# Performance work log

Measured on AMD Instinct MI355X. Metric: run time of the kernel, lower is better.

## Reference

```python
import jax, jax.numpy as jnp
import numpy as np

T, N, G, H, E = 20, 256, 8, 128, 64
G2 = G * G


def setup_inputs() -> dict:
    key = jax.random.key(0)
    ks = jax.random.split(key, 16)
    scene = jax.random.normal(ks[0], (T, N, 3), dtype=jnp.float32)
    grids = (jax.random.uniform(ks[1], (T, N, N, G2)) < 0.05).astype(jnp.float32)
    hidden_states = jax.random.normal(ks[2], (N, H), dtype=jnp.float32) * 0.1
    cell_states = jax.random.normal(ks[3], (N, H), dtype=jnp.float32) * 0.1
    dimensions = jnp.array([640, 480], dtype=jnp.int64)
    s = lambda fan: 1.0 / np.sqrt(fan)
    W_in = jax.random.normal(ks[4], (E, 2), dtype=jnp.float32) * s(2)
    b_in = jnp.zeros((E,), dtype=jnp.float32)
    W_t = jax.random.normal(ks[5], (E, G2 * H), dtype=jnp.float32) * s(G2 * H)
    b_t = jnp.zeros((E,), dtype=jnp.float32)
    W_ih = jax.random.normal(ks[6], (4 * H, 2 * E), dtype=jnp.float32) * s(2 * E)
    b_ih = jnp.zeros((4 * H,), dtype=jnp.float32)
    W_hh = jax.random.normal(ks[7], (4 * H, H), dtype=jnp.float32) * s(H)
    b_hh = jnp.zeros((4 * H,), dtype=jnp.float32)
    W_out = jax.random.normal(ks[8], (5, H), dtype=jnp.float32) * s(H)
    b_out = jnp.zeros((5,), dtype=jnp.float32)
    return {"scene": scene, "grids": grids, "hidden_states": hidden_states,
            "cell_states": cell_states, "dimensions": dimensions,
            "W_in": W_in, "b_in": b_in, "W_t": W_t, "b_t": b_t,
            "W_ih": W_ih, "b_ih": b_ih, "W_hh": W_hh, "b_hh": b_hh,
            "W_out": W_out, "b_out": b_out}


def reference(scene, grids, hidden_states, cell_states, dimensions,
              W_in, b_in, W_t, b_t, W_ih, b_ih, W_hh, b_hh, W_out, b_out):
    # dimensions is unused by forward() (only by infer()), kept for signature fidelity.
    xy_seq = scene[:, :, 1:3]  # [T, N, 2]

    def step(carry, xs):
        h, c = carry                      # [N, H] each
        xy, grid = xs                     # [N, 2], [N, N, G2]
        # social pooling: for each ped p, grid[p]^T @ h  -> [G2, H]
        social = jnp.einsum('pog,oh->pgh', grid, h).reshape(grid.shape[0], G2 * H)
        inp_emb = jax.nn.relu(xy @ W_in.T + b_in)         # [N, E] (dropout in eval mode)
        ten_emb = jax.nn.relu(social @ W_t.T + b_t)       # [N, E]
        x = jnp.concatenate([inp_emb, ten_emb], axis=1)   # [N, 2E]
        gates = x @ W_ih.T + b_ih + h @ W_hh.T + b_hh     # [N, 4H]
        i, f, g, o = jnp.split(gates, 4, axis=1)          # PyTorch LSTMCell gate order
        c2 = jax.nn.sigmoid(f) * c + jax.nn.sigmoid(i) * jnp.tanh(g)
        h2 = jax.nn.sigmoid(o) * jnp.tanh(c2)
        out = h2 @ W_out.T + b_out                        # [N, 5]
        return (h2, c2), out

    (h_fin, c_fin), outputs = jax.lax.scan(step, (hidden_states, cell_states), (xy_seq, grids))
    return outputs, h_fin, c_fin
```

## Files before the change

### kernel.cpp

```cpp
#include <hip/hip_runtime.h>
#include <cstdint>
#include <cstddef>

#define T_STEPS 20
#define N_PED   256
#define G2C     64
#define HDIM    128
#define EDIM    64
#define NG      16384

__device__ __forceinline__ int swz(int row, int hd) {
    return row * 128 + ((((hd >> 2) ^ (row & 31)) << 2) | (hd & 3));
}

__global__ __launch_bounds__(256) void kP(
    const float* __restrict__ scene, const float* __restrict__ hidden,
    const float* __restrict__ cell,  const float* __restrict__ W_in,
    const float* __restrict__ b_in,  const float* __restrict__ W_ih,
    const float* __restrict__ b_ih,  const float* __restrict__ b_hh,
    float* __restrict__ pg, float* __restrict__ h0, float* __restrict__ c0,
    float* __restrict__ W_ihT)
{
    int bid = blockIdx.x, tid = threadIdx.x;
    if (bid >= 1280) {
        int gid = (bid - 1280) * 256 + tid;
        for (int u = gid; u < 32768; u += 4096) {
            h0[u] = hidden[u];
            c0[u] = cell[u];
            int e = u >> 9, j = u & 511;
            W_ihT[u] = W_ih[j * 128 + 64 + e];
        }
        return;
    }
    __shared__ float ie[16 * 64];
    __shared__ float wih[128 * 65];
    int tb = bid >> 6;
    int p0 = ((bid >> 2) & 15) * 16;
    int j0 = (bid & 3) * 128;

    for (int k = 0; k < 8; ++k) {
        int f4 = tid + k * 256;
        int fl = f4 * 4;
        int j_loc = fl >> 6, e0 = fl & 63;
        float4 v = *(const float4*)(W_ih + (size_t)(j0 + j_loc) * 128 + e0);
        wih[j_loc * 65 + e0 + 0] = v.x;
        wih[j_loc * 65 + e0 + 1] = v.y;
        wih[j_loc * 65 + e0 + 2] = v.z;
        wih[j_loc * 65 + e0 + 3] = v.w;
    }
    {
        int pp = tid >> 4, e0 = (tid & 15) * 4;
        size_t sbase = ((size_t)tb * N_PED + (p0 + pp)) * 3;
        float x = scene[sbase + 1];
        float y = scene[sbase + 2];
        #pragma unroll
        for (int i = 0; i < 4; ++i) {
            int e = e0 + i;
            float v = b_in[e] + x * W_in[e * 2 + 0] + y * W_in[e * 2 + 1];
            ie[pp * 64 + e] = v > 0.f ? v : 0.f;
        }
    }
    __syncthreads();
    for (int k = 0; k < 8; ++k) {
        int u = k * 256 + tid;
        int pp = u >> 7, j_loc = u & 127;
        int j = j0 + j_loc;
        float s = b_ih[j] + b_hh[j];
        #pragma unroll 8
        for (int e = 0; e < 64; ++e)
            s = fmaf(ie[pp * 64 + e], wih[j_loc * 65 + e], s);
        pg[((size_t)tb * N_PED + (p0 + pp)) * 512 + j] = s;
    }
}

__global__ __launch_bounds__(256) void kC(
    const float* __restrict__ grids, int* __restrict__ counts,
    unsigned short* __restrict__ gidx)
{
    int r = blockIdx.x;
    int tid = threadIdx.x, lane = tid & 63, w = tid >> 6;
    __shared__ unsigned short st[4][1024];
    __shared__ int wcnts[4];
    const float* row = grids + (size_t)r * NG;
    int wcnt = 0;
    for (int rd = 0; rd < 16; ++rd) {
        int fb = w * 4096 + rd * 256 + lane * 4;
        float4 v = *(const float4*)(row + fb);
        #pragma unroll
        for (int c = 0; c < 4; ++c) {
            float val = (c == 0) ? v.x : (c == 1) ? v.y : (c == 2) ? v.z : v.w;
            unsigned long long m = __ballot(val != 0.0f);
            if (val != 0.0f) {
                int pos = wcnt + (int)__popcll(m & ((1ull << lane) - 1ull));
                st[w][pos] = (unsigned short)(fb + c);
            }
            wcnt += (int)__popcll(m);
        }
    }
    if (lane == 0) wcnts[w] = wcnt;
    __syncthreads();
    int base = 0;
    #pragma unroll
    for (int i = 0; i < 4; ++i) if (i < w) base += wcnts[i];
    for (int k = lane; k < wcnt; k += 64)
        gidx[(size_t)r * 1024 + base + k] = st[w][k];
    if (tid == 0) counts[r] = wcnts[0] + wcnts[1] + wcnts[2] + wcnts[3];
}

__global__ __launch_bounds__(256) void k1(
    const float* __restrict__ h, const float* __restrict__ W_t,
    const float* __restrict__ W_hh, float* __restrict__ A,
    float* __restrict__ hhg)
{
    __shared__ float smem[16384];
    float* hs = smem;
    float* wt = smem + 8192;
    int bid = blockIdx.x, tid = threadIdx.x;

    if (bid < 256) {
        int g = bid & 63, o0 = (bid >> 6) * 64;
        for (int k = 0; k < 8; ++k) {
            int fl = (tid + k * 256) * 4;
            int r = fl >> 7, hd = fl & 127;
            float4 v = *(const float4*)(h + (size_t)(o0 + r) * 128 + hd);
            *(float4*)&hs[swz(r, hd)] = v;
            float4 wv = *(const float4*)(W_t + (size_t)r * 8192 + g * 128 + hd);
            *(float4*)&wt[swz(r, hd)] = wv;
        }
        __syncthreads();
        int o_l = (tid >> 4) * 4, e_l = (tid & 15) * 4;
        float acc[4][4] = {};
        for (int hb = 0; hb < 32; ++hb) {
            int hd = hb << 2;
            float4 a[4], b[4];
            #pragma unroll
            for (int i = 0; i < 4; ++i) a[i] = *(float4*)&hs[swz(o_l + i, hd)];
            #pragma unroll
            for (int j = 0; j < 4; ++j) b[j] = *(float4*)&wt[swz(e_l + j, hd)];
            #pragma unroll
            for (int i = 0; i < 4; ++i)
                #pragma unroll
                for (int j = 0; j < 4; ++j) {
                    acc[i][j] = fmaf(a[i].x, b[j].x, acc[i][j]);
                    acc[i][j] = fmaf(a[i].y, b[j].y, acc[i][j]);
                    acc[i][j] = fmaf(a[i].z, b[j].z, acc[i][j]);
                    acc[i][j] = fmaf(a[i].w, b[j].w, acc[i][j]);
                }
        }
        #pragma unroll
        for (int i = 0; i < 4; ++i) {
            float4 r4 = make_float4(acc[i][0], acc[i][1], acc[i][2], acc[i][3]);
            *(float4*)&A[(size_t)(o0 + o_l + i) * 4096 + g * 64 + e_l] = r4;
        }
    } else {
        int hb2 = bid - 256;
        int o0 = (hb2 & 3) * 64, j0 = (hb2 >> 2) * 32;
        for (int k = 0; k < 8; ++k) {
            int fl = (tid + k * 256) * 4;
            int r = fl >> 7, hd = fl & 127;
            float4 v = *(const float4*)(h + (size_t)(o0 + r) * 128 + hd);
            *(float4*)&hs[swz(r, hd)] = v;
        }
        for (int k = 0; k < 4; ++k) {
            int fl = (tid + k * 256) * 4;
            int r = fl >> 7, hd = fl & 127;
            float4 wv = *(const float4*)(W_hh + (size_t)(j0 + r) * 128 + hd);
            *(float4*)&wt[swz(r, hd)] = wv;
        }
        __syncthreads();
        int o_l = (tid >> 4) * 4, j_l = (tid & 15) * 2;
        float acc[4][2] = {};
        for (int hb = 0; hb < 32; ++hb) {
            int hd = hb << 2;
            float4 a[4], b[2];
            #pragma unroll
            for (int i = 0; i < 4; ++i) a[i] = *(float4*)&hs[swz(o_l + i, hd)];
            #pragma unroll
            for (int j = 0; j < 2; ++j) b[j] = *(float4*)&wt[swz(j_l + j, hd)];
            #pragma unroll
            for (int i = 0; i < 4; ++i)
                #pragma unroll
                for (int j = 0; j < 2; ++j) {
                    acc[i][j] = fmaf(a[i].x, b[j].x, acc[i][j]);
                    acc[i][j] = fmaf(a[i].y, b[j].y, acc[i][j]);
                    acc[i][j] = fmaf(a[i].z, b[j].z, acc[i][j]);
                    acc[i][j] = fmaf(a[i].w, b[j].w, acc[i][j]);
                }
        }
        #pragma unroll
        for (int i = 0; i < 4; ++i) {
            float2 r2 = make_float2(acc[i][0], acc[i][1]);
            *(float2*)&hhg[(size_t)(o0 + o_l + i) * 512 + j0 + j_l] = r2;
        }
    }
}

__global__ __launch_bounds__(512) void k2(
    int t, int last, const int* __restrict__ counts,
    const unsigned short* __restrict__ gidx,
    const float* __restrict__ A,     const float* __restrict__ hhg,
    const float* __restrict__ pg,    const float* __restrict__ W_ihT,
    const float* __restrict__ b_t,   const float* __restrict__ W_out,
    const float* __restrict__ b_out, const float* __restrict__ c_cur,
    float* __restrict__ c_next, float* __restrict__ h_next,
    float* __restrict__ out)
{
    int p = blockIdx.x;
    int tid = threadIdx.x, lane = tid & 63, w = tid >> 6;
    __shared__ unsigned short lidx[1024];
    __shared__ float part[8][64];
    __shared__ float ten[64];
    __shared__ float gts[512];
    __shared__ float h2s[128];

    int r = t * N_PED + p;
    int cnt = counts[r];
    ((unsigned int*)lidx)[tid] = ((const unsigned int*)(gidx + (size_t)r * 1024))[tid];
    __syncthreads();

    float acc = 0.f;
    int k = w;
    for (; k + 24 < cnt; k += 32) {
        int i0 = lidx[k], i1 = lidx[k + 8], i2 = lidx[k + 16], i3 = lidx[k + 24];
        float a0 = A[(size_t)i0 * 64 + lane];
        float a1 = A[(size_t)i1 * 64 + lane];
        float a2 = A[(size_t)i2 * 64 + lane];
        float a3 = A[(size_t)i3 * 64 + lane];
        acc += a0; acc += a1; acc += a2; acc += a3;
    }
    for (; k < cnt; k += 8)
        acc += A[(size_t)lidx[k] * 64 + lane];
    part[w][lane] = acc;
    __syncthreads();

    if (tid < 64) {
        float s = b_t[tid];
        #pragma unroll
        for (int ww = 0; ww < 8; ++ww) s += part[ww][tid];
        ten[tid] = s > 0.f ? s : 0.f;
    }
    __syncthreads();

    {
        int j = tid;
        float gj = pg[(size_t)r * 512 + j] + hhg[(size_t)p * 512 + j];
        #pragma unroll 8
        for (int e = 0; e < 64; ++e)
            gj = fmaf(ten[e], W_ihT[e * 512 + j], gj);
        gts[j] = gj;
    }
    __syncthreads();

    if (tid < 128) {
        float ig = gts[tid], fg = gts[128 + tid], gg = gts[256 + tid], og = gts[384 + tid];
        float si = 1.f / (1.f + expf(-ig));
        float sf = 1.f / (1.f + expf(-fg));
        float so = 1.f / (1.f + expf(-og));
        float cold = c_cur[p * 128 + tid];
        float c2 = sf * cold + si * tanhf(gg);
        float h2 = so * tanhf(c2);
        c_next[p * 128 + tid] = c2;
        h_next[p * 128 + tid] = h2;
        h2s[tid] = h2;
        if (last) {
            out[25600 + p * 128 + tid] = h2;
            out[58368 + p * 128 + tid] = c2;
        }
    }
    __syncthreads();

    if (w < 5) {
        float s = h2s[lane] * W_out[w * 128 + lane]
                + h2s[lane + 64] * W_out[w * 128 + 64 + lane];
        #pragma unroll
        for (int off = 32; off > 0; off >>= 1) s += __shfl_xor(s, off);
        if (lane == 0) out[(size_t)r * 5 + w] = s + b_out[w];
    }
}

extern "C" void kernel_launch(void* const* d_in, const int* in_sizes, int n_in,
                              void* d_out, int out_size, void* d_ws, size_t ws_size,
                              hipStream_t stream) {
    (void)in_sizes; (void)n_in; (void)out_size; (void)ws_size;
    const float* scene  = (const float*)d_in[0];
    const float* grids  = (const float*)d_in[1];
    const float* hidden = (const float*)d_in[2];
    const float* cell   = (const float*)d_in[3];
    const float* W_in  = (const float*)d_in[5];
    const float* b_in  = (const float*)d_in[6];
    const float* W_t   = (const float*)d_in[7];
    const float* b_t   = (const float*)d_in[8];
    const float* W_ih  = (const float*)d_in[9];
    const float* b_ih  = (const float*)d_in[10];
    const float* W_hh  = (const float*)d_in[11];
    const float* b_hh  = (const float*)d_in[12];
    const float* W_out = (const float*)d_in[13];
    const float* b_out = (const float*)d_in[14];

    float* ws   = (float*)d_ws;
    float* hbuf = ws;
    float* cbuf = ws + 65536;
    float* A    = ws + 131072;
    float* hhg  = ws + 1179648;
    float* pg   = ws + 1310720;
    float* WT   = ws + 3932160;
    int*   counts = (int*)(ws + 3964928);
    unsigned short* gidx = (unsigned short*)(ws + 3970048);
    float* outf = (float*)d_out;

    hipLaunchKernelGGL(kC, dim3(5120), dim3(256), 0, stream,
                       grids, counts, gidx);
    hipLaunchKernelGGL(kP, dim3(1296), dim3(256), 0, stream,
                       scene, hidden, cell, W_in, b_in, W_ih, b_ih, b_hh,
                       pg, hbuf, cbuf, WT);

    for (int t = 0; t < T_STEPS; ++t) {
        const float* hcur = hbuf + (t & 1) * 32768;
        float*       hnxt = hbuf + ((t + 1) & 1) * 32768;
        const float* ccur = cbuf + (t & 1) * 32768;
        float*       cnxt = cbuf + ((t + 1) & 1) * 32768;
        hipLaunchKernelGGL(k1, dim3(320), dim3(256), 0, stream,
                           hcur, W_t, W_hh, A, hhg);
        hipLaunchKernelGGL(k2, dim3(256), dim3(512), 0, stream,
                           t, (t == T_STEPS - 1) ? 1 : 0,
                           counts, gidx, A, hhg, pg, WT, b_t, W_out, b_out,
                           ccur, cnxt, hnxt, outf);
    }
}
```

Measured before the change: 1.067 ms.

## Fuse per-timestep kernels into one persistent cooperative kernel with grid sync

Replaces the 40 per-step launches (k1 projection GEMM and k2 gather/LSTM) with a single cooperative kernel that loops over all timesteps and separates phases with grid-wide syncs. The h@W_hh term moves from a separate GEMM into the per-pedestrian gate loop, using a W_hhT transposed in the prep kernel. The A GEMM splits the K dimension across warp halves and reduces through shared memory. This is meant to remove launch overhead and inter-kernel gaps, at the cost of grid-sync latency and fewer blocks (256) doing the A GEMM.

New measurement: 2.235 ms. 110% more time.

```diff
diff --git a/kernel.cpp b/kernel.cpp
--- a/kernel.cpp
+++ b/kernel.cpp
@@ -1,16 +1,16 @@
 #include <hip/hip_runtime.h>
+#include <hip/hip_cooperative_groups.h>
 #include <cstdint>
 #include <cstddef>
 
+namespace cg = cooperative_groups;
+
 #define T_STEPS 20
 #define N_PED   256
-#define G2C     64
-#define HDIM    128
-#define EDIM    64
 #define NG      16384
 
-__device__ __forceinline__ int swz(int row, int hd) {
-    return row * 128 + ((((hd >> 2) ^ (row & 31)) << 2) | (hd & 3));
+__device__ __forceinline__ int swz64(int row, int k) {
+    return row * 64 + ((((k >> 2) ^ (row & 15)) << 2) | (k & 3));
 }
 
 __global__ __launch_bounds__(256) void kP(
@@ -18,8 +18,9 @@
     const float* __restrict__ cell,  const float* __restrict__ W_in,
     const float* __restrict__ b_in,  const float* __restrict__ W_ih,
     const float* __restrict__ b_ih,  const float* __restrict__ b_hh,
+    const float* __restrict__ W_hh,
     float* __restrict__ pg, float* __restrict__ h0, float* __restrict__ c0,
-    float* __restrict__ W_ihT)
+    float* __restrict__ W_ihT, float* __restrict__ W_hhT)
 {
     int bid = blockIdx.x, tid = threadIdx.x;
     if (bid >= 1280) {
@@ -30,6 +31,10 @@
             int e = u >> 9, j = u & 511;
             W_ihT[u] = W_ih[j * 128 + 64 + e];
         }
+        for (int u = gid; u < 65536; u += 4096) {
+            int h = u >> 9, j = u & 511;
+            W_hhT[u] = W_hh[j * 128 + h];
+        }
         return;
     }
     __shared__ float ie[16 * 64];
@@ -39,8 +44,7 @@
     int j0 = (bid & 3) * 128;
 
     for (int k = 0; k < 8; ++k) {
-        int f4 = tid + k * 256;
-        int fl = f4 * 4;
+        int fl = (tid + k * 256) * 4;
         int j_loc = fl >> 6, e0 = fl & 63;
         float4 v = *(const float4*)(W_ih + (size_t)(j0 + j_loc) * 128 + e0);
         wih[j_loc * 65 + e0 + 0] = v.x;
@@ -107,174 +111,168 @@
     if (tid == 0) counts[r] = wcnts[0] + wcnts[1] + wcnts[2] + wcnts[3];
 }
 
-__global__ __launch_bounds__(256) void k1(
-    const float* __restrict__ h, const float* __restrict__ W_t,
-    const float* __restrict__ W_hh, float* __restrict__ A,
-    float* __restrict__ hhg)
+__global__ __launch_bounds__(512) void kStep(
+    const int* __restrict__ counts, const unsigned short* __restrict__ gidx,
+    const float* __restrict__ W_t,  const float* __restrict__ pg,
+    const float* __restrict__ W_ihT, const float* __restrict__ W_hhT,
+    const float* __restrict__ b_t,  const float* __restrict__ W_out,
+    const float* __restrict__ b_out,
+    float* __restrict__ hbuf, float* __restrict__ cbuf,
+    float* __restrict__ A, float* __restrict__ out)
 {
+    cg::grid_group gg = cg::this_grid();
     __shared__ float smem[16384];
-    float* hs = smem;
-    float* wt = smem + 8192;
     int bid = blockIdx.x, tid = threadIdx.x;
-
-    if (bid < 256) {
-        int g = bid & 63, o0 = (bid >> 6) * 64;
-        for (int k = 0; k < 8; ++k) {
-            int fl = (tid + k * 256) * 4;
-            int r = fl >> 7, hd = fl & 127;
-            float4 v = *(const float4*)(h + (size_t)(o0 + r) * 128 + hd);
-            *(float4*)&hs[swz(r, hd)] = v;
-            float4 wv = *(const float4*)(W_t + (size_t)r * 8192 + g * 128 + hd);
-            *(float4*)&wt[swz(r, hd)] = wv;
-        }
-        __syncthreads();
-        int o_l = (tid >> 4) * 4, e_l = (tid & 15) * 4;
-        float acc[4][4] = {};
-        for (int hb = 0; hb < 32; ++hb) {
-            int hd = hb << 2;
-            float4 a[4], b[4];
+    int lane = tid & 63, w = tid >> 6;
+
+    for (int t = 0; t < T_STEPS; ++t) {
+        const float* h  = hbuf + (t & 1) * 32768;
+        const float* c  = cbuf + (t & 1) * 32768;
+        float*       hn = hbuf + ((t + 1) & 1) * 32768;
+        float*       cn = cbuf + ((t + 1) & 1) * 32768;
+
+        {
+            int o0 = (bid >> 6) * 64, g = bid & 63;
             #pragma unroll
-            for (int i = 0; i < 4; ++i) a[i] = *(float4*)&hs[swz(o_l + i, hd)];
+            for (int i = 0; i < 8; ++i) {
+                int u = i * 512 + tid;
+                if (u < 2048) {
+                    int kh = u >> 10, rem = u & 1023, r = rem >> 4, k4 = (rem & 15) * 4;
+                    float4 v = *(const float4*)(h + (size_t)(o0 + r) * 128 + kh * 64 + k4);
+                    *(float4*)&smem[kh * 4096 + swz64(r, k4)] = v;
+                } else {
+                    int v2 = u - 2048;
+                    int kh = v2 >> 10, rem = v2 & 1023, e = rem >> 4, k4 = (rem & 15) * 4;
+                    float4 v = *(const float4*)(W_t + (size_t)e * 8192 + g * 128 + kh * 64 + k4);
+                    *(float4*)&smem[8192 + kh * 4096 + swz64(e, k4)] = v;
+                }
+            }
+            __syncthreads();
+            int kh = w >> 2, wq = w & 3;
+            int wrow = (wq >> 1) * 32, wcol = (wq & 1) * 32;
+            int lr = (lane >> 3) * 4, lc = (lane & 7) * 4;
+            const float* hsb = &smem[kh * 4096];
+            const float* wtb = &smem[8192 + kh * 4096];
+            float acc[4][4] = {};
             #pragma unroll
-            for (int j = 0; j < 4; ++j) b[j] = *(float4*)&wt[swz(e_l + j, hd)];
-            #pragma unroll
-            for (int i = 0; i < 4; ++i)
-                #pragma unroll
-                for (int j = 0; j < 4; ++j) {
-                    acc[i][j] = fmaf(a[i].x, b[j].x, acc[i][j]);
-                    acc[i][j] = fmaf(a[i].y, b[j].y, acc[i][j]);
-                    acc[i][j] = fmaf(a[i].z, b[j].z, acc[i][j]);
-                    acc[i][j] = fmaf(a[i].w, b[j].w, acc[i][j]);
+            for (int k4i = 0; k4i < 16; ++k4i) {
+                int kd = k4i * 4;
+                float4 a[4], b[4];
+                #pragma unroll
+                for (int i = 0; i < 4; ++i) a[i] = *(const float4*)&hsb[swz64(wrow + lr + i, kd)];
+                #pragma unroll
+                for (int j = 0; j < 4; ++j) b[j] = *(const float4*)&wtb[swz64(wcol + lc + j, kd)];
+                #pragma unroll
+                for (int i = 0; i < 4; ++i)
+                    #pragma unroll
+                    for (int j = 0; j < 4; ++j) {
+                        acc[i][j] = fmaf(a[i].x, b[j].x, acc[i][j]);
+                        acc[i][j] = fmaf(a[i].y, b[j].y, acc[i][j]);
+                        acc[i][j] = fmaf(a[i].z, b[j].z, acc[i][j]);
+                        acc[i][j] = fmaf(a[i].w, b[j].w, acc[i][j]);
+                    }
+            }
+            __syncthreads();
+            if (kh == 1) {
+                #pragma unroll
+                for (int i = 0; i < 4; ++i) {
+                    int row = wrow + lr + i;
+                    int col = (wcol + lc) ^ (((row >> 2) & 7) << 3);
+                    *(float4*)&smem[row * 64 + col] =
+                        make_float4(acc[i][0], acc[i][1], acc[i][2], acc[i][3]);
                 }
-        }
-        #pragma unroll
-        for (int i = 0; i < 4; ++i) {
-            float4 r4 = make_float4(acc[i][0], acc[i][1], acc[i][2], acc[i][3]);
-            *(float4*)&A[(size_t)(o0 + o_l + i) * 4096 + g * 64 + e_l] = r4;
-        }
-    } else {
-        int hb2 = bid - 256;
-        int o0 = (hb2 & 3) * 64, j0 = (hb2 >> 2) * 32;
-        for (int k = 0; k < 8; ++k) {
-            int fl = (tid + k * 256) * 4;
-            int r = fl >> 7, hd = fl & 127;
-            float4 v = *(const float4*)(h + (size_t)(o0 + r) * 128 + hd);
-            *(float4*)&hs[swz(r, hd)] = v;
-        }
-        for (int k = 0; k < 4; ++k) {
-            int fl = (tid + k * 256) * 4;
-            int r = fl >> 7, hd = fl & 127;
-            float4 wv = *(const float4*)(W_hh + (size_t)(j0 + r) * 128 + hd);
-            *(float4*)&wt[swz(r, hd)] = wv;
-        }
-        __syncthreads();
-        int o_l = (tid >> 4) * 4, j_l = (tid & 15) * 2;
-        float acc[4][2] = {};
-        for (int hb = 0; hb < 32; ++hb) {
-            int hd = hb << 2;
-            float4 a[4], b[2];
-            #pragma unroll
-            for (int i = 0; i < 4; ++i) a[i] = *(float4*)&hs[swz(o_l + i, hd)];
-            #pragma unroll
-            for (int j = 0; j < 2; ++j) b[j] = *(float4*)&wt[swz(j_l + j, hd)];
-            #pragma unroll
-            for (int i = 0; i < 4; ++i)
-                #pragma unroll
-                for (int j = 0; j < 2; ++j) {
-                    acc[i][j] = fmaf(a[i].x, b[j].x, acc[i][j]);
-                    acc[i][j] = fmaf(a[i].y, b[j].y, acc[i][j]);
-                    acc[i][j] = fmaf(a[i].z, b[j].z, acc[i][j]);
-                    acc[i][j] = fmaf(a[i].w, b[j].w, acc[i][j]);
+            }
+            __syncthreads();
+            if (kh == 0) {
+                #pragma unroll
+                for (int i = 0; i < 4; ++i) {
+                    int row = wrow + lr + i;
+                    int col = (wcol + lc) ^ (((row >> 2) & 7) << 3);
+                    float4 r4 = *(const float4*)&smem[row * 64 + col];
+                    float4 o4 = make_float4(acc[i][0] + r4.x, acc[i][1] + r4.y,
+                                            acc[i][2] + r4.z, acc[i][3] + r4.w);
+                    *(float4*)&A[(size_t)(o0 + row) * 4096 + g * 64 + wcol + lc] = o4;
                 }
-        }
-        #pragma unroll
-        for (int i = 0; i < 4; ++i) {
-            float2 r2 = make_float2(acc[i][0], acc[i][1]);
-            *(float2*)&hhg[(size_t)(o0 + o_l + i) * 512 + j0 + j_l] = r2;
-        }
-    }
-}
-
-__global__ __launch_bounds__(512) void k2(
-    int t, int last, const int* __restrict__ counts,
-    const unsigned short* __restrict__ gidx,
-    const float* __restrict__ A,     const float* __restrict__ hhg,
-    const float* __restrict__ pg,    const float* __restrict__ W_ihT,
-    const float* __restrict__ b_t,   const float* __restrict__ W_out,
-    const float* __restrict__ b_out, const float* __restrict__ c_cur,
-    float* __restrict__ c_next, float* __restrict__ h_next,
-    float* __restrict__ out)
-{
-    int p = blockIdx.x;
-    int tid = threadIdx.x, lane = tid & 63, w = tid >> 6;
-    __shared__ unsigned short lidx[1024];
-    __shared__ float part[8][64];
-    __shared__ float ten[64];
-    __shared__ float gts[512];
-    __shared__ float h2s[128];
-
-    int r = t * N_PED + p;
-    int cnt = counts[r];
-    ((unsigned int*)lidx)[tid] = ((const unsigned int*)(gidx + (size_t)r * 1024))[tid];
-    __syncthreads();
-
-    float acc = 0.f;
-    int k = w;
-    for (; k + 24 < cnt; k += 32) {
-        int i0 = lidx[k], i1 = lidx[k + 8], i2 = lidx[k + 16], i3 = lidx[k + 24];
-        float a0 = A[(size_t)i0 * 64 + lane];
-        float a1 = A[(size_t)i1 * 64 + lane];
-        float a2 = A[(size_t)i2 * 64 + lane];
-        float a3 = A[(size_t)i3 * 64 + lane];
-        acc += a0; acc += a1; acc += a2; acc += a3;
-    }
-    for (; k < cnt; k += 8)
-        acc += A[(size_t)lidx[k] * 64 + lane];
-    part[w][lane] = acc;
-    __syncthreads();
-
-    if (tid < 64) {
-        float s = b_t[tid];
-        #pragma unroll
-        for (int ww = 0; ww < 8; ++ww) s += part[ww][tid];
-        ten[tid] = s > 0.f ? s : 0.f;
-    }
-    __syncthreads();
-
-    {
-        int j = tid;
-        float gj = pg[(size_t)r * 512 + j] + hhg[(size_t)p * 512 + j];
-        #pragma unroll 8
-        for (int e = 0; e < 64; ++e)
-            gj = fmaf(ten[e], W_ihT[e * 512 + j], gj);
-        gts[j] = gj;
-    }
-    __syncthreads();
-
-    if (tid < 128) {
-        float ig = gts[tid], fg = gts[128 + tid], gg = gts[256 + tid], og = gts[384 + tid];
-        float si = 1.f / (1.f + expf(-ig));
-        float sf = 1.f / (1.f + expf(-fg));
-        float so = 1.f / (1.f + expf(-og));
-        float cold = c_cur[p * 128 + tid];
-        float c2 = sf * cold + si * tanhf(gg);
-        float h2 = so * tanhf(c2);
-        c_next[p * 128 + tid] = c2;
-        h_next[p * 128 + tid] = h2;
-        h2s[tid] = h2;
-        if (last) {
-            out[25600 + p * 128 + tid] = h2;
-            out[58368 + p * 128 + tid] = c2;
-        }
-    }
-    __syncthreads();
-
-    if (w < 5) {
-        float s = h2s[lane] * W_out[w * 128 + lane]
-                + h2s[lane + 64] * W_out[w * 128 + 64 + lane];
-        #pragma unroll
-        for (int off = 32; off > 0; off >>= 1) s += __shfl_xor(s, off);
-        if (lane == 0) out[(size_t)r * 5 + w] = s + b_out[w];
+            }
+        }
+        gg.sync();
+
+        {
+            int p = bid, r = t * N_PED + p;
+            unsigned short* lidx = (unsigned short*)smem;
+            float* part = smem + 512;
+            float* ten  = smem + 1024;
+            float* gts  = smem + 1088;
+            float* h2s  = smem + 1600;
+            float* hcur = smem + 1728;
+            int cnt = counts[r];
+            ((unsigned int*)lidx)[tid] = ((const unsigned int*)(gidx + (size_t)r * 1024))[tid];
+            if (tid < 128) hcur[tid] = h[p * 128 + tid];
+            __syncthreads();
+
+            float acc = 0.f;
+            int k = w;
+            for (; k + 24 < cnt; k += 32) {
+                int i0 = lidx[k], i1 = lidx[k + 8], i2 = lidx[k + 16], i3 = lidx[k + 24];
+                float a0 = A[(size_t)i0 * 64 + lane];
+                float a1 = A[(size_t)i1 * 64 + lane];
+                float a2 = A[(size_t)i2 * 64 + lane];
+                float a3 = A[(size_t)i3 * 64 + lane];
+                acc += a0; acc += a1; acc += a2; acc += a3;
+            }
+            for (; k < cnt; k += 8)
+                acc += A[(size_t)lidx[k] * 64 + lane];
+            part[w * 64 + lane] = acc;
+            __syncthreads();
+
+            if (tid < 64) {
+                float s = b_t[tid];
+                #pragma unroll
+                for (int ww = 0; ww < 8; ++ww) s += part[ww * 64 + tid];
+                ten[tid] = s > 0.f ? s : 0.f;
+            }
+            __syncthreads();
+
+            {
+                int j = tid;
+                float gj = pg[(size_t)r * 512 + j];
+                #pragma unroll 8
+                for (int e = 0; e < 64; ++e)
+                    gj = fmaf(ten[e], W_ihT[e * 512 + j], gj);
+                #pragma unroll 8
+                for (int hd = 0; hd < 128; ++hd)
+                    gj = fmaf(hcur[hd], W_hhT[hd * 512 + j], gj);
+                gts[j] = gj;
+            }
+            __syncthreads();
+
+            if (tid < 128) {
+                float ig = gts[tid], fg = gts[128 + tid], ggt = gts[256 + tid], og = gts[384 + tid];
+                float si = 1.f / (1.f + expf(-ig));
+                float sf = 1.f / (1.f + expf(-fg));
+                float so = 1.f / (1.f + expf(-og));
+                float cold = c[p * 128 + tid];
+                float c2 = sf * cold + si * tanhf(ggt);
+                float h2 = so * tanhf(c2);
+                cn[p * 128 + tid] = c2;
+                hn[p * 128 + tid] = h2;
+                h2s[tid] = h2;
+                if (t == T_STEPS - 1) {
+                    out[25600 + p * 128 + tid] = h2;
+                    out[58368 + p * 128 + tid] = c2;
+                }
+            }
+            __syncthreads();
+
+            if (w < 5) {
+                float s = h2s[lane] * W_out[w * 128 + lane]
+                        + h2s[lane + 64] * W_out[w * 128 + 64 + lane];
+                #pragma unroll
+                for (int off = 32; off > 0; off >>= 1) s += __shfl_xor(s, off);
+                if (lane == 0) out[(size_t)r * 5 + w] = s + b_out[w];
+            }
+        }
+        gg.sync();
     }
 }
 
@@ -301,29 +299,29 @@
     float* hbuf = ws;
     float* cbuf = ws + 65536;
     float* A    = ws + 131072;
-    float* hhg  = ws + 1179648;
     float* pg   = ws + 1310720;
     float* WT   = ws + 3932160;
     int*   counts = (int*)(ws + 3964928);
     unsigned short* gidx = (unsigned short*)(ws + 3970048);
+    float* W_hhT = ws + 6591488;
     float* outf = (float*)d_out;
 
     hipLaunchKernelGGL(kC, dim3(5120), dim3(256), 0, stream,
                        grids, counts, gidx);
     hipLaunchKernelGGL(kP, dim3(1296), dim3(256), 0, stream,
-                       scene, hidden, cell, W_in, b_in, W_ih, b_ih, b_hh,
-                       pg, hbuf, cbuf, WT);
-
-    for (int t = 0; t < T_STEPS; ++t) {
-        const float* hcur = hbuf + (t & 1) * 32768;
-        float*       hnxt = hbuf + ((t + 1) & 1) * 32768;
-        const float* ccur = cbuf + (t & 1) * 32768;
-        float*       cnxt = cbuf + ((t + 1) & 1) * 32768;
-        hipLaunchKernelGGL(k1, dim3(320), dim3(256), 0, stream,
-                           hcur, W_t, W_hh, A, hhg);
-        hipLaunchKernelGGL(k2, dim3(256), dim3(512), 0, stream,
-                           t, (t == T_STEPS - 1) ? 1 : 0,
-                           counts, gidx, A, hhg, pg, WT, b_t, W_out, b_out,
-                           ccur, cnxt, hnxt, outf);
-    }
-}
+                       scene, hidden, cell, W_in, b_in, W_ih, b_ih, b_hh, W_hh,
+                       pg, hbuf, cbuf, WT, W_hhT);
+
+    const int* counts_c = counts;
+    const unsigned short* gidx_c = gidx;
+    const float* WT_c = WT;
+    const float* W_hhT_c = W_hhT;
+    const float* pg_c = pg;
+    void* args[] = {
+        (void*)&counts_c, (void*)&gidx_c, (void*)&W_t, (void*)&pg_c,
+        (void*)&WT_c, (void*)&W_hhT_c, (void*)&b_t, (void*)&W_out,
+        (void*)&b_out, (void*)&hbuf, (void*)&cbuf, (void*)&A, (void*)&outf
+    };
+    hipLaunchCooperativeKernel((const void*)kStep, dim3(256), dim3(512),
+                               args, 0, stream);
+}
```
